# Optimization experiments

Hardware: AMD Instinct MI355X
Metric: run time of the kernel (lower is better)

Reference implementation:

```python
import jax, jax.numpy as jnp
import numpy as np

N = 20000      # nodes
DEG = 16       # out-degree per node
E = N * DEG    # edges
DIM = 128
H = 8          # heads
HD = DIM // H  # head_dim = 16
HE = 8         # expanded_heads = int(1.0 * H)
SCALE = HD ** -0.5


def setup_inputs() -> dict:
    key = jax.random.key(0)
    ks = jax.random.split(key, 10)
    s = 0.05
    x = jax.random.normal(ks[0], (N, DIM), jnp.float32)
    edges = jax.random.normal(ks[1], (E, DIM), jnp.float32)
    # unique structured edges: src i -> dst (i+1..i+DEG) mod N (no duplicates, no self-loops)
    src = jnp.repeat(jnp.arange(N, dtype=jnp.int32), DEG)
    off = jnp.tile(jnp.arange(1, DEG + 1, dtype=jnp.int32), N)
    dst = (src + off) % N
    edge_index = jnp.stack([src, dst], axis=0)
    Wq = jax.random.normal(ks[2], (DIM, DIM), jnp.float32) * s
    Wk = jax.random.normal(ks[3], (DIM, DIM), jnp.float32) * s
    Wv = jax.random.normal(ks[4], (DIM, HE * HD), jnp.float32) * s
    Wek = jax.random.normal(ks[5], (DIM, DIM), jnp.float32) * s
    Wev = jax.random.normal(ks[6], (DIM, HE * HD), jnp.float32) * s
    Wexp = jax.random.normal(ks[7], (H, HE), jnp.float32) * s
    Wout = jax.random.normal(ks[8], (HE * HD, DIM), jnp.float32) * s
    bout = jnp.zeros((DIM,), jnp.float32)
    return {"x": x, "edges": edges, "edge_index": edge_index,
            "Wq": Wq, "Wk": Wk, "Wv": Wv, "Wek": Wek, "Wev": Wev,
            "Wexp": Wexp, "Wout": Wout, "bout": bout}


def reference(x, edges, edge_index, Wq, Wk, Wv, Wek, Wev, Wexp, Wout, bout):
    n = x.shape[0]
    src, dst = edge_index[0], edge_index[1]
    # per-edge gathered q, k(+edge_k): [E, H, HD]
    qg = (x @ Wq)[src].reshape(-1, H, HD)
    kg = ((x @ Wk)[dst] * SCALE + (edges @ Wek) * SCALE).reshape(-1, H, HD)
    scores = jnp.einsum('ehd,ehd->eh', qg, kg)        # [E, H]
    scores = scores @ Wexp                             # head expansion -> [E, HE]
    # segment softmax over destination dim per src node (matches dense masked softmax:
    # non-edge entries exp(-fmax - max) == 0 in fp32; row sum / degree D[n] == 1)
    seg_max = jax.ops.segment_max(scores, src, num_segments=n)   # [N, HE]
    exps = jnp.exp(scores - seg_max[src])
    denom = jax.ops.segment_sum(exps, src, num_segments=n)       # [N, HE]
    a = exps / denom[src]                                        # [E, HE]
    # values with edge bias: [E, HE, HD]
    v_e = ((x @ Wv)[dst] + edges @ Wev).reshape(-1, HE, HD)
    # Laplacian contraction: out[n] = D[n]*v_square[n,n] - sum_e a_e * v_e, D[n]=1
    agg = jax.ops.segment_sum(a[:, :, None] * v_e, src, num_segments=n)  # [N, HE, HD]
    self_m = (src == dst).astype(x.dtype)
    self_c = jax.ops.segment_sum(v_e * self_m[:, None, None], src, num_segments=n)
    out = (self_c - agg).reshape(n, HE * HD)
    return out @ Wout + bout
```

## Files before the change

### kernel.cpp

```cpp
#include <hip/hip_runtime.h>


#define N_NODES 20000
#define DEG     16
#define E_EDGES (N_NODES * DEG)
#define SCALE   0.25f
#define KV_ROWS 19
#define KV_LD   132

typedef __attribute__((ext_vector_type(8))) short short8;
typedef __attribute__((ext_vector_type(4))) float f32x4;

__device__ __forceinline__ short f2bf(float f) {
  unsigned u = __builtin_bit_cast(unsigned, f);
  u += 0x7fffu + ((u >> 16) & 1u);
  return (short)(u >> 16);
}
__device__ __forceinline__ short8 pack8(float4 a, float4 b) {
  short8 r;
  r[0] = f2bf(a.x); r[1] = f2bf(a.y); r[2] = f2bf(a.z); r[3] = f2bf(a.w);
  r[4] = f2bf(b.x); r[5] = f2bf(b.y); r[6] = f2bf(b.z); r[7] = f2bf(b.w);
  return r;
}

__global__ __launch_bounds__(128) void k_prep(
    const float* __restrict__ Wq, const float* __restrict__ Wk,
    const float* __restrict__ Wv, const float* __restrict__ Wek,
    const float* __restrict__ Wev, const float* __restrict__ Wout,
    unsigned short* __restrict__ Wcat_t, unsigned short* __restrict__ Wekv_t,
    unsigned short* __restrict__ Wout_t) {
  const int r = blockIdx.x;
  const int k = threadIdx.x;
  float v;
  unsigned short* dst;
  if (r < 384) {
    if (r < 128)      v = Wq[k * 128 + r] * SCALE;
    else if (r < 256) v = Wk[k * 128 + (r - 128)];
    else              v = Wv[k * 128 + (r - 256)];
    dst = Wcat_t + r * 128 + k;
  } else if (r < 640) {
    const int n = r - 384;
    v = (n < 128) ? Wek[k * 128 + n] : Wev[k * 128 + (n - 128)];
    dst = Wekv_t + n * 128 + k;
  } else {
    const int n = r - 640;
    v = Wout[k * 128 + n];
    dst = Wout_t + n * 128 + k;
  }
  *dst = (unsigned short)f2bf(v);
}

__global__ __launch_bounds__(256) void k_nodeproj(
    const float* __restrict__ x, const unsigned short* __restrict__ Wcat_t,
    float* __restrict__ qkv) {
  const int t = threadIdx.x, lane = t & 63, wave = t >> 6;
  const int lo = lane & 15, hi = lane >> 4;
  const int n0 = blockIdx.x * 16;

  short8 b[6][4];
  const unsigned short* wb = Wcat_t + (size_t)(wave * 96 + lo) * 128 + hi * 8;
#pragma unroll
  for (int nt = 0; nt < 6; ++nt)
#pragma unroll
    for (int ks = 0; ks < 4; ++ks)
      b[nt][ks] = *(const short8*)(wb + nt * 16 * 128 + ks * 32);

  const float* ax = x + (size_t)(n0 + lo) * 128 + hi * 8;
  short8 a[4];
#pragma unroll
  for (int ks = 0; ks < 4; ++ks) {
    float4 f0 = *(const float4*)(ax + ks * 32);
    float4 f1 = *(const float4*)(ax + ks * 32 + 4);
    a[ks] = pack8(f0, f1);
  }

  f32x4 acc[6];
#pragma unroll
  for (int nt = 0; nt < 6; ++nt) acc[nt] = (f32x4){0.f, 0.f, 0.f, 0.f};
#pragma unroll
  for (int nt = 0; nt < 6; ++nt)
#pragma unroll
    for (int ks = 0; ks < 4; ++ks)
      acc[nt] = __builtin_amdgcn_mfma_f32_16x16x32_bf16(a[ks], b[nt][ks], acc[nt], 0, 0, 0);

#pragma unroll
  for (int nt = 0; nt < 6; ++nt) {
    const int col = wave * 96 + nt * 16 + lo;
#pragma unroll
    for (int r = 0; r < 4; ++r)
      qkv[(size_t)(n0 + hi * 4 + r) * 384 + col] = acc[nt][r];
  }
}

#define SM_K(r, c) smem[(r) * KV_LD + (c)]
#define SM_V(r, c) smem[KV_ROWS * KV_LD + (r) * KV_LD + (c)]
#define SM_Q(r, c) smem[2 * KV_ROWS * KV_LD + (r) * 128 + (c)]
#define SM_TOTAL   (2 * KV_ROWS * KV_LD + 4 * 128)

__global__ __launch_bounds__(256) void k_edge_attn(
    const float* __restrict__ edges, const int* __restrict__ ei,
    const unsigned short* __restrict__ Wekv_t, const float* __restrict__ Wexp,
    const unsigned short* __restrict__ Wout_t, const float* __restrict__ bout,
    const float* __restrict__ qkv, float* __restrict__ out) {
  __shared__ float smem[SM_TOTAL];
  __shared__ float o_lds[4][KV_LD];
  __shared__ float s_sc[64][8];
  __shared__ float s_a[64][8];
  __shared__ int   s_dst[64];
  __shared__ float s_self[64];

  const int t = threadIdx.x, lane = t & 63, wave = t >> 6;
  const int lo = lane & 15, hi = lane >> 4;
  const int n0 = blockIdx.x * 4;
  const int e0 = blockIdx.x * 64;

  float4 stg[6];
  int    soff[6];
#pragma unroll
  for (int i = 0; i < 6; ++i) {
    const int idx = t + i * 256;
    if (idx < 1344) {
      const float* src;
      int off;
      if (idx < 1216) {
        const int half = (idx >= 608);
        const int j = idx - half * 608;
        const int r = j >> 5, c = (j & 31) << 2;
        int d = n0 + 1 + r; if (d >= N_NODES) d -= N_NODES;
        src = qkv + (size_t)d * 384 + 128 + half * 128 + c;
        off = half * (KV_ROWS * KV_LD) + r * KV_LD + c;
      } else {
        const int j = idx - 1216;
        const int r = j >> 5, c = (j & 31) << 2;
        src = qkv + (size_t)(n0 + r) * 384 + c;
        off = 2 * KV_ROWS * KV_LD + r * 128 + c;
      }
      soff[i] = off;
      stg[i] = *(const float4*)src;
    } else {
      soff[i] = -1;
      stg[i] = (float4){0.f, 0.f, 0.f, 0.f};
    }
  }
  int srcv = 0, dstv = 0;
  if (t < 64) {
    srcv = ei[e0 + t];
    dstv = ei[E_EDGES + e0 + t];
  }

  short8 b[4][4];
  const unsigned short* wb = Wekv_t + (size_t)(wave * 64 + lo) * 128 + hi * 8;
#pragma unroll
  for (int nt = 0; nt < 4; ++nt)
#pragma unroll
    for (int ks = 0; ks < 4; ++ks)
      b[nt][ks] = *(const short8*)(wb + nt * 16 * 128 + ks * 32);

  f32x4 acc[4][4];
#pragma unroll
  for (int mt = 0; mt < 4; ++mt)
#pragma unroll
    for (int nt = 0; nt < 4; ++nt) acc[mt][nt] = (f32x4){0.f, 0.f, 0.f, 0.f};

#pragma unroll
  for (int mt = 0; mt < 4; ++mt) {
    const float* ae = edges + (size_t)(e0 + mt * 16 + lo) * 128 + hi * 8;
    short8 a[4];
#pragma unroll
    for (int ks = 0; ks < 4; ++ks) {
      float4 f0 = *(const float4*)(ae + ks * 32);
      float4 f1 = *(const float4*)(ae + ks * 32 + 4);
      a[ks] = pack8(f0, f1);
    }
#pragma unroll
    for (int nt = 0; nt < 4; ++nt)
#pragma unroll
      for (int ks = 0; ks < 4; ++ks)
        acc[mt][nt] = __builtin_amdgcn_mfma_f32_16x16x32_bf16(a[ks], b[nt][ks], acc[mt][nt], 0, 0, 0);
  }

#pragma unroll
  for (int i = 0; i < 6; ++i)
    if (soff[i] >= 0) *(float4*)&smem[soff[i]] = stg[i];
  if (t < 64) {
    s_dst[t]  = dstv;
    s_self[t] = (srcv == dstv) ? 1.f : 0.f;
  }
  __syncthreads();

  if (wave < 2) {
#pragma unroll
    for (int mt = 0; mt < 4; ++mt) {
      int li_[4];
#pragma unroll
      for (int r = 0; r < 4; ++r) {
        const int d = s_dst[mt * 16 + hi * 4 + r];
        int li = d - n0 - 1; if (li < 0) li += N_NODES;
        li_[r] = li;
      }
#pragma unroll
      for (int nt = 0; nt < 4; ++nt) {
        const int col = wave * 64 + nt * 16 + lo;
        const int h   = wave * 4 + nt;
        const float q = SM_Q(mt, col);
#pragma unroll
        for (int r = 0; r < 4; ++r) {
          float p = q * (SM_K(li_[r], col) + acc[mt][nt][r]);
          p += __shfl_xor(p, 1);
          p += __shfl_xor(p, 2);
          p += __shfl_xor(p, 4);
          p += __shfl_xor(p, 8);
          if (lo == 0) s_sc[mt * 16 + hi * 4 + r][h] = p;
        }
      }
    }
  }
  __syncthreads();

  if (t < 32) {
    const int nb = t >> 3, he = t & 7;
    float we[8];
#pragma unroll
    for (int hh = 0; hh < 8; ++hh) we[hh] = Wexp[hh * 8 + he];
    float sc[16];
    float m = -1e30f;
#pragma unroll
    for (int j = 0; j < 16; ++j) {
      float v = 0.f;
#pragma unroll
      for (int hh = 0; hh < 8; ++hh) v += s_sc[nb * 16 + j][hh] * we[hh];
      sc[j] = v;
      m = fmaxf(m, v);
    }
    float sum = 0.f;
#pragma unroll
    for (int j = 0; j < 16; ++j) { sc[j] = __expf(sc[j] - m); sum += sc[j]; }
    const float inv = 1.f / sum;
#pragma unroll
    for (int j = 0; j < 16; ++j) s_a[nb * 16 + j][he] = sc[j] * inv;
  }
  __syncthreads();

  if (wave >= 2) {
#pragma unroll
    for (int mt = 0; mt < 4; ++mt) {
      int li_[4];
#pragma unroll
      for (int r = 0; r < 4; ++r) {
        const int d = s_dst[mt * 16 + hi * 4 + r];
        int li = d - n0 - 1; if (li < 0) li += N_NODES;
        li_[r] = li;
      }
#pragma unroll
      for (int nt = 0; nt < 4; ++nt) {
        const int cv = (wave - 2) * 64 + nt * 16 + lo;
        const int he = (wave - 2) * 4 + nt;
        float og = 0.f;
#pragma unroll
        for (int r = 0; r < 4; ++r) {
          const int e = mt * 16 + hi * 4 + r;
          const float coef = s_self[e] - s_a[e][he];
          og += coef * (SM_V(li_[r], cv) + acc[mt][nt][r]);
        }
        og += __shfl_xor(og, 16);
        og += __shfl_xor(og, 32);
        if (hi == 0) o_lds[mt][cv] = og;
      }
    }
  }
  __syncthreads();

  short8 bo[2][4];
  const unsigned short* wo = Wout_t + (size_t)(wave * 32 + lo) * 128 + hi * 8;
#pragma unroll
  for (int nt = 0; nt < 2; ++nt)
#pragma unroll
    for (int ks = 0; ks < 4; ++ks)
      bo[nt][ks] = *(const short8*)(wo + nt * 16 * 128 + ks * 32);
  float bias[2];
#pragma unroll
  for (int nt = 0; nt < 2; ++nt) bias[nt] = bout[wave * 32 + nt * 16 + lo];

  short8 af[4];
  if (lo < 4) {
#pragma unroll
    for (int ks = 0; ks < 4; ++ks) {
      float4 f0 = *(const float4*)&o_lds[lo][ks * 32 + hi * 8];
      float4 f1 = *(const float4*)&o_lds[lo][ks * 32 + hi * 8 + 4];
      af[ks] = pack8(f0, f1);
    }
  } else {
    const short8 z = {0, 0, 0, 0, 0, 0, 0, 0};
#pragma unroll
    for (int ks = 0; ks < 4; ++ks) af[ks] = z;
  }

  f32x4 acc2[2];
  acc2[0] = (f32x4){0.f, 0.f, 0.f, 0.f};
  acc2[1] = (f32x4){0.f, 0.f, 0.f, 0.f};
#pragma unroll
  for (int nt = 0; nt < 2; ++nt)
#pragma unroll
    for (int ks = 0; ks < 4; ++ks)
      acc2[nt] = __builtin_amdgcn_mfma_f32_16x16x32_bf16(af[ks], bo[nt][ks], acc2[nt], 0, 0, 0);

  if (hi == 0) {
#pragma unroll
    for (int nt = 0; nt < 2; ++nt) {
      const int colo = wave * 32 + nt * 16 + lo;
#pragma unroll
      for (int r = 0; r < 4; ++r)
        out[(size_t)(n0 + r) * 128 + colo] = acc2[nt][r] + bias[nt];
    }
  }
}

extern "C" void kernel_launch(void* const* d_in, const int* in_sizes, int n_in,
                              void* d_out, int out_size, void* d_ws, size_t ws_size,
                              hipStream_t stream) {
  const float* x     = (const float*)d_in[0];
  const float* edges = (const float*)d_in[1];
  const int*   ei    = (const int*)  d_in[2];
  const float* Wq    = (const float*)d_in[3];
  const float* Wk    = (const float*)d_in[4];
  const float* Wv    = (const float*)d_in[5];
  const float* Wek   = (const float*)d_in[6];
  const float* Wev   = (const float*)d_in[7];
  const float* Wexp  = (const float*)d_in[8];
  const float* Wout  = (const float*)d_in[9];
  const float* bout  = (const float*)d_in[10];
  float* out = (float*)d_out;

  unsigned short* Wcat_t = (unsigned short*)d_ws;
  unsigned short* Wekv_t = Wcat_t + (size_t)384 * 128;
  unsigned short* Wout_t = Wekv_t + (size_t)256 * 128;
  float*          qkv    = (float*)(Wout_t + (size_t)128 * 128);

  k_prep<<<dim3(768), dim3(128), 0, stream>>>(Wq, Wk, Wv, Wek, Wev, Wout,
                                              Wcat_t, Wekv_t, Wout_t);
  k_nodeproj<<<dim3(N_NODES / 16), dim3(256), 0, stream>>>(x, Wcat_t, qkv);
  k_edge_attn<<<dim3(N_NODES / 4), dim3(256), 0, stream>>>(edges, ei, Wekv_t,
                                                           Wexp, Wout_t, bout,
                                                           qkv, out);
}
```

Baseline: 502.1 us.

## Assign one node per wave, load K/V/Q via global_load_lds, swizzle block order

Restructures the edge-attention kernel so each wave owns one source node's 16 edges and computes all 16 output tiles (K and V projections) for them. The scores, softmax and aggregation then run per wave with no block barriers in between. K/V/Q rows are staged directly into LDS with global_load_lds instead of going through registers. The block index is swizzled across 8 groups. The cost is that each wave now reads the full Wekv matrix from global or cache, raising weight traffic and register pressure with 16 accumulators. The K/V LDS rows are no longer padded, so bank conflicts may increase.

```diff
diff --git a/kernel.cpp b/kernel.cpp
--- a/kernel.cpp
+++ b/kernel.cpp
@@ -5,8 +5,6 @@
 #define DEG     16
 #define E_EDGES (N_NODES * DEG)
 #define SCALE   0.25f
-#define KV_ROWS 19
-#define KV_LD   132
 
 typedef __attribute__((ext_vector_type(8))) short short8;
 typedef __attribute__((ext_vector_type(4))) float f32x4;
@@ -92,181 +90,149 @@
   }
 }
 
-#define SM_K(r, c) smem[(r) * KV_LD + (c)]
-#define SM_V(r, c) smem[KV_ROWS * KV_LD + (r) * KV_LD + (c)]
-#define SM_Q(r, c) smem[2 * KV_ROWS * KV_LD + (r) * 128 + (c)]
-#define SM_TOTAL   (2 * KV_ROWS * KV_LD + 4 * 128)
+#define KF_K 0
+#define KF_V 2432
+#define KF_Q 4864
+#define SMF  5376
 
 __global__ __launch_bounds__(256) void k_edge_attn(
     const float* __restrict__ edges, const int* __restrict__ ei,
     const unsigned short* __restrict__ Wekv_t, const float* __restrict__ Wexp,
     const unsigned short* __restrict__ Wout_t, const float* __restrict__ bout,
     const float* __restrict__ qkv, float* __restrict__ out) {
-  __shared__ float smem[SM_TOTAL];
-  __shared__ float o_lds[4][KV_LD];
-  __shared__ float s_sc[64][8];
-  __shared__ float s_a[64][8];
+  __shared__ float smem[SMF];
+  __shared__ float o_lds[4][132];
+  __shared__ float s_sc[4][16][8];
+  __shared__ float s_a[4][16][8];
   __shared__ int   s_dst[64];
   __shared__ float s_self[64];
 
   const int t = threadIdx.x, lane = t & 63, wave = t >> 6;
   const int lo = lane & 15, hi = lane >> 4;
-  const int n0 = blockIdx.x * 4;
-  const int e0 = blockIdx.x * 64;
-
-  float4 stg[6];
-  int    soff[6];
-#pragma unroll
-  for (int i = 0; i < 6; ++i) {
-    const int idx = t + i * 256;
-    if (idx < 1344) {
-      const float* src;
-      int off;
-      if (idx < 1216) {
-        const int half = (idx >= 608);
-        const int j = idx - half * 608;
-        const int r = j >> 5, c = (j & 31) << 2;
-        int d = n0 + 1 + r; if (d >= N_NODES) d -= N_NODES;
-        src = qkv + (size_t)d * 384 + 128 + half * 128 + c;
-        off = half * (KV_ROWS * KV_LD) + r * KV_LD + c;
-      } else {
-        const int j = idx - 1216;
-        const int r = j >> 5, c = (j & 31) << 2;
-        src = qkv + (size_t)(n0 + r) * 384 + c;
-        off = 2 * KV_ROWS * KV_LD + r * 128 + c;
-      }
-      soff[i] = off;
-      stg[i] = *(const float4*)src;
+  int bid = blockIdx.x;
+  bid = (bid & 7) * (N_NODES / 4 / 8) + (bid >> 3);
+  const int n0  = bid * 4;
+  const int e0  = bid * 64;
+  const int nw  = n0 + wave;
+  const int e0w = nw * 16;
+
+  for (int i = wave; i < 21; i += 4) {
+    const int idx = i * 64 + lane;
+    const float* src;
+    if (idx < 608) {
+      int d = n0 + 1 + (idx >> 5); if (d >= N_NODES) d -= N_NODES;
+      src = qkv + (size_t)d * 384 + 128 + (idx & 31) * 4;
+    } else if (idx < 1216) {
+      const int j = idx - 608;
+      int d = n0 + 1 + (j >> 5); if (d >= N_NODES) d -= N_NODES;
+      src = qkv + (size_t)d * 384 + 256 + (j & 31) * 4;
     } else {
-      soff[i] = -1;
-      stg[i] = (float4){0.f, 0.f, 0.f, 0.f};
-    }
-  }
+      const int j = idx - 1216;
+      src = qkv + (size_t)(n0 + (j >> 5)) * 384 + (j & 31) * 4;
+    }
+    __builtin_amdgcn_global_load_lds(
+        (const __attribute__((address_space(1))) unsigned int*)src,
+        (__attribute__((address_space(3))) unsigned int*)&smem[i * 256],
+        16, 0, 0);
+  }
+
   int srcv = 0, dstv = 0;
   if (t < 64) {
     srcv = ei[e0 + t];
     dstv = ei[E_EDGES + e0 + t];
   }
 
-  short8 b[4][4];
-  const unsigned short* wb = Wekv_t + (size_t)(wave * 64 + lo) * 128 + hi * 8;
-#pragma unroll
-  for (int nt = 0; nt < 4; ++nt)
-#pragma unroll
-    for (int ks = 0; ks < 4; ++ks)
-      b[nt][ks] = *(const short8*)(wb + nt * 16 * 128 + ks * 32);
-
-  f32x4 acc[4][4];
-#pragma unroll
-  for (int mt = 0; mt < 4; ++mt)
-#pragma unroll
-    for (int nt = 0; nt < 4; ++nt) acc[mt][nt] = (f32x4){0.f, 0.f, 0.f, 0.f};
-
-#pragma unroll
-  for (int mt = 0; mt < 4; ++mt) {
-    const float* ae = edges + (size_t)(e0 + mt * 16 + lo) * 128 + hi * 8;
-    short8 a[4];
+  const int he0 = lane & 7;
+  float we[8];
+#pragma unroll
+  for (int h = 0; h < 8; ++h) we[h] = Wexp[h * 8 + he0];
+
+  const float* ae = edges + (size_t)(e0w + lo) * 128 + hi * 8;
+  short8 a[4];
+#pragma unroll
+  for (int ks = 0; ks < 4; ++ks) {
+    float4 f0 = *(const float4*)(ae + ks * 32);
+    float4 f1 = *(const float4*)(ae + ks * 32 + 4);
+    a[ks] = pack8(f0, f1);
+  }
+
+  f32x4 acc[16];
+#pragma unroll
+  for (int nt = 0; nt < 16; ++nt) acc[nt] = (f32x4){0.f, 0.f, 0.f, 0.f};
+  const unsigned short* wbase = Wekv_t + (size_t)lo * 128 + hi * 8;
+#pragma unroll
+  for (int nt = 0; nt < 16; ++nt) {
+    const unsigned short* wp = wbase + nt * 16 * 128;
 #pragma unroll
     for (int ks = 0; ks < 4; ++ks) {
-      float4 f0 = *(const float4*)(ae + ks * 32);
-      float4 f1 = *(const float4*)(ae + ks * 32 + 4);
-      a[ks] = pack8(f0, f1);
-    }
-#pragma unroll
-    for (int nt = 0; nt < 4; ++nt)
-#pragma unroll
-      for (int ks = 0; ks < 4; ++ks)
-        acc[mt][nt] = __builtin_amdgcn_mfma_f32_16x16x32_bf16(a[ks], b[nt][ks], acc[mt][nt], 0, 0, 0);
-  }
-
-#pragma unroll
-  for (int i = 0; i < 6; ++i)
-    if (soff[i] >= 0) *(float4*)&smem[soff[i]] = stg[i];
+      const short8 b = *(const short8*)(wp + ks * 32);
+      acc[nt] = __builtin_amdgcn_mfma_f32_16x16x32_bf16(a[ks], b, acc[nt], 0, 0, 0);
+    }
+  }
+
   if (t < 64) {
     s_dst[t]  = dstv;
     s_self[t] = (srcv == dstv) ? 1.f : 0.f;
   }
   __syncthreads();
 
-  if (wave < 2) {
-#pragma unroll
-    for (int mt = 0; mt < 4; ++mt) {
-      int li_[4];
-#pragma unroll
-      for (int r = 0; r < 4; ++r) {
-        const int d = s_dst[mt * 16 + hi * 4 + r];
-        int li = d - n0 - 1; if (li < 0) li += N_NODES;
-        li_[r] = li;
-      }
-#pragma unroll
-      for (int nt = 0; nt < 4; ++nt) {
-        const int col = wave * 64 + nt * 16 + lo;
-        const int h   = wave * 4 + nt;
-        const float q = SM_Q(mt, col);
-#pragma unroll
-        for (int r = 0; r < 4; ++r) {
-          float p = q * (SM_K(li_[r], col) + acc[mt][nt][r]);
-          p += __shfl_xor(p, 1);
-          p += __shfl_xor(p, 2);
-          p += __shfl_xor(p, 4);
-          p += __shfl_xor(p, 8);
-          if (lo == 0) s_sc[mt * 16 + hi * 4 + r][h] = p;
-        }
-      }
-    }
-  }
-  __syncthreads();
-
-  if (t < 32) {
-    const int nb = t >> 3, he = t & 7;
-    float we[8];
-#pragma unroll
-    for (int hh = 0; hh < 8; ++hh) we[hh] = Wexp[hh * 8 + he];
-    float sc[16];
-    float m = -1e30f;
-#pragma unroll
-    for (int j = 0; j < 16; ++j) {
-      float v = 0.f;
-#pragma unroll
-      for (int hh = 0; hh < 8; ++hh) v += s_sc[nb * 16 + j][hh] * we[hh];
-      sc[j] = v;
-      m = fmaxf(m, v);
-    }
-    float sum = 0.f;
-#pragma unroll
-    for (int j = 0; j < 16; ++j) { sc[j] = __expf(sc[j] - m); sum += sc[j]; }
-    const float inv = 1.f / sum;
-#pragma unroll
-    for (int j = 0; j < 16; ++j) s_a[nb * 16 + j][he] = sc[j] * inv;
-  }
-  __syncthreads();
-
-  if (wave >= 2) {
-#pragma unroll
-    for (int mt = 0; mt < 4; ++mt) {
-      int li_[4];
-#pragma unroll
-      for (int r = 0; r < 4; ++r) {
-        const int d = s_dst[mt * 16 + hi * 4 + r];
-        int li = d - n0 - 1; if (li < 0) li += N_NODES;
-        li_[r] = li;
-      }
-#pragma unroll
-      for (int nt = 0; nt < 4; ++nt) {
-        const int cv = (wave - 2) * 64 + nt * 16 + lo;
-        const int he = (wave - 2) * 4 + nt;
-        float og = 0.f;
-#pragma unroll
-        for (int r = 0; r < 4; ++r) {
-          const int e = mt * 16 + hi * 4 + r;
-          const float coef = s_self[e] - s_a[e][he];
-          og += coef * (SM_V(li_[r], cv) + acc[mt][nt][r]);
-        }
-        og += __shfl_xor(og, 16);
-        og += __shfl_xor(og, 32);
-        if (hi == 0) o_lds[mt][cv] = og;
-      }
-    }
+  int li_[4];
+#pragma unroll
+  for (int r = 0; r < 4; ++r) {
+    const int d = s_dst[wave * 16 + hi * 4 + r];
+    int li = d - n0 - 1; if (li < 0) li += N_NODES;
+    li_[r] = li;
+  }
+
+#pragma unroll
+  for (int h = 0; h < 8; ++h) {
+    const float q = smem[KF_Q + wave * 128 + h * 16 + lo];
+#pragma unroll
+    for (int r = 0; r < 4; ++r) {
+      float p = q * (smem[KF_K + li_[r] * 128 + h * 16 + lo] + acc[h][r]);
+      p += __shfl_xor(p, 1);
+      p += __shfl_xor(p, 2);
+      p += __shfl_xor(p, 4);
+      p += __shfl_xor(p, 8);
+      if (lo == 0) s_sc[wave][hi * 4 + r][h] = p;
+    }
+  }
+
+  const int ep = lane >> 3;
+  float v0 = 0.f, v1 = 0.f;
+#pragma unroll
+  for (int h = 0; h < 8; ++h) {
+    v0 += s_sc[wave][ep][h]     * we[h];
+    v1 += s_sc[wave][ep + 8][h] * we[h];
+  }
+  float m = fmaxf(v0, v1);
+  m = fmaxf(m, __shfl_xor(m, 8));
+  m = fmaxf(m, __shfl_xor(m, 16));
+  m = fmaxf(m, __shfl_xor(m, 32));
+  const float ex0 = __expf(v0 - m), ex1 = __expf(v1 - m);
+  float s = ex0 + ex1;
+  s += __shfl_xor(s, 8);
+  s += __shfl_xor(s, 16);
+  s += __shfl_xor(s, 32);
+  const float inv = 1.f / s;
+  s_a[wave][ep][he0]     = ex0 * inv;
+  s_a[wave][ep + 8][he0] = ex1 * inv;
+
+  float sf[4];
+#pragma unroll
+  for (int r = 0; r < 4; ++r) sf[r] = s_self[wave * 16 + hi * 4 + r];
+#pragma unroll
+  for (int nt = 0; nt < 8; ++nt) {
+    const int cv = nt * 16 + lo;
+    float og = 0.f;
+#pragma unroll
+    for (int r = 0; r < 4; ++r) {
+      const float coef = sf[r] - s_a[wave][hi * 4 + r][nt];
+      og += coef * (smem[KF_V + li_[r] * 128 + cv] + acc[8 + nt][r]);
+    }
+    og += __shfl_xor(og, 16);
+    og += __shfl_xor(og, 32);
+    if (hi == 0) o_lds[wave][cv] = og;
   }
   __syncthreads();
 
```

New measurement: 484.5 us. 3.5% less time.
